# Kernel tuning notes

Hardware: AMD Instinct MI355X
Metric: run time of the kernel (lower is better)

## Reference

```python
import jax, jax.numpy as jnp
import numpy as np

N, B, C, H = 1024, 4, 1024, 8
D = C // H  # head dim = 128


def setup_inputs() -> dict:
    key = jax.random.key(0)
    ks = jax.random.split(key, 10)
    f = lambda k, s: jax.random.normal(k, s, dtype=jnp.float32)
    w = lambda k: f(k, (C, C)) * 0.02  # torch Linear weight layout (out, in)
    return {
        "query_reg": f(ks[0], (N, B, C)),
        "key_reg": f(ks[1], (N, B, C)),
        "query_cls": f(ks[2], (N, B, C)),
        "key_cls": f(ks[3], (N, B, C)),
        "value": f(ks[4], (N, B, C)),
        "W_q_reg": w(ks[5]),
        "W_k_reg": w(ks[6]),
        "W_q_cls": w(ks[7]),
        "W_k_cls": w(ks[8]),
        "W_v": w(ks[9]),
    }


def _proj_heads(x, W):
    # x: (N, B, C); torch Linear: y = x @ W.T -> reshape (N,B,H,D) -> (B,H,N,D)
    y = jnp.einsum('nbc,dc->nbd', x, W)
    return y.reshape(N, B, H, D).transpose(1, 2, 0, 3)


def _l2norm(x):
    return x / jnp.linalg.norm(x, axis=-1, keepdims=True)


def reference(query_reg, key_reg, query_cls, key_cls, value,
              W_q_reg, W_k_reg, W_q_cls, W_k_cls, W_v):
    q_reg = _l2norm(_proj_heads(query_reg, W_q_reg))  # (B,H,N,D)
    k_reg = _l2norm(_proj_heads(key_reg, W_k_reg))
    q_cls = _l2norm(_proj_heads(query_cls, W_q_cls))
    k_cls = _l2norm(_proj_heads(key_cls, W_k_cls))
    v = _proj_heads(value, W_v)

    attn_reg = jax.nn.softmax(jnp.einsum('bhnd,bhmd->bhnm', q_reg, k_reg), axis=-1)
    attn_cls = jax.nn.softmax(jnp.einsum('bhnd,bhmd->bhnm', q_cls, k_cls), axis=-1)
    attn = (attn_reg + attn_cls) * 0.5  # (B,H,N,N)

    x = jnp.einsum('bhnm,bhmd->bhnd', attn, v)  # (B,H,N,D)
    x = x.transpose(0, 2, 1, 3).reshape(B, N, C)  # (B,N,C)
    return (x.transpose(1, 0, 2), attn)  # ((N,B,C), (B,H,N,N))
```

## Files before the change

kernel.cpp:

```cpp
#include <hip/hip_runtime.h>

#define DEVINL __device__ __forceinline__

typedef unsigned short u16;
typedef float f32x4 __attribute__((ext_vector_type(4)));
typedef __bf16 bf16x8 __attribute__((ext_vector_type(8)));

constexpr int N_ = 1024, B_ = 4, C_ = 1024, H_ = 8, D_ = 128;
constexpr int NB = N_ * B_;
constexpr int BH = B_ * H_;

DEVINL u16 f2bf(float f) {
  unsigned u = __builtin_bit_cast(unsigned, f);
  u += 0x7fffu + ((u >> 16) & 1u);
  return (u16)(u >> 16);
}

typedef __attribute__((address_space(1))) void gv_t;
typedef __attribute__((address_space(3))) void lv_t;
DEVINL void gload16(const void* g, void* l) {
  __builtin_amdgcn_global_load_lds((gv_t*)(unsigned long long)g,
                                   (lv_t*)(unsigned)(unsigned long long)l, 16, 0, 0);
}
DEVINL bf16x8 ld_frag(const u16* p) { return *(const bf16x8*)p; }
DEVINL f32x4 mfma16(bf16x8 a, bf16x8 b, f32x4 c) {
  return __builtin_amdgcn_mfma_f32_16x16x32_bf16(a, b, c, 0, 0, 0);
}

struct ConvArgs { const float* s[10]; u16* d[10]; int n[10]; };

__global__ __launch_bounds__(256) void k_convert(ConvArgs a) {
  const int which = blockIdx.y;
  const int i = (blockIdx.x * 256 + threadIdx.x) * 8;
  if (i >= a.n[which]) return;
  const float* s = a.s[which] + i;
  float4 v0 = *(const float4*)s;
  float4 v1 = *(const float4*)(s + 4);
  union { uint4 v; u16 r[8]; } u;
  u.r[0] = f2bf(v0.x); u.r[1] = f2bf(v0.y); u.r[2] = f2bf(v0.z); u.r[3] = f2bf(v0.w);
  u.r[4] = f2bf(v1.x); u.r[5] = f2bf(v1.y); u.r[6] = f2bf(v1.z); u.r[7] = f2bf(v1.w);
  *(uint4*)(a.d[which] + i) = u.v;
}

struct ProjArgs { const u16* X[5]; const u16* W[5]; u16* O[5]; };

__global__ __launch_bounds__(256) void k_proj(ProjArgs a) {
  __shared__ u16 lA[128 * 64];
  __shared__ u16 lB[128 * 64];
  __shared__ float lred[128][2];
  const int tid = threadIdx.x, w = tid >> 6, lane = tid & 63;
  const int qd = lane >> 4, m16 = lane & 15;
  const int wr = w >> 1, wc = w & 1;
  const int r0 = blockIdx.y * 128, d0 = blockIdx.x * 128;
  const u16* __restrict__ X = a.X[blockIdx.z];
  const u16* __restrict__ W = a.W[blockIdx.z];
  u16* __restrict__ O = a.O[blockIdx.z];
  const bool donorm = blockIdx.z < 4;

  f32x4 acc[4][4];
  const f32x4 fz = {0.f, 0.f, 0.f, 0.f};
#pragma unroll
  for (int i = 0; i < 4; ++i)
#pragma unroll
    for (int j = 0; j < 4; ++j) acc[i][j] = fz;

  for (int k0 = 0; k0 < C_; k0 += 64) {
    __syncthreads();
#pragma unroll
    for (int i = 0; i < 4; ++i) {
      int p = i * 256 + tid, row = p >> 3, cp = p & 7, cl = cp ^ (row & 7);
      gload16(X + (size_t)(r0 + row) * C_ + k0 + cl * 8, &lA[p * 8]);
    }
#pragma unroll
    for (int i = 0; i < 4; ++i) {
      int p = i * 256 + tid, row = p >> 3, cp = p & 7, cl = cp ^ (row & 7);
      gload16(W + (size_t)(d0 + row) * C_ + k0 + cl * 8, &lB[p * 8]);
    }
    __syncthreads();
#pragma unroll
    for (int ks = 0; ks < 2; ++ks) {
      bf16x8 af[4], bfr[4];
#pragma unroll
      for (int t = 0; t < 4; ++t) {
        int row = wr * 64 + t * 16 + m16;
        af[t] = ld_frag(&lA[row * 64 + (((ks * 4 + qd) ^ (row & 7)) * 8)]);
        int col = wc * 64 + t * 16 + m16;
        bfr[t] = ld_frag(&lB[col * 64 + (((ks * 4 + qd) ^ (col & 7)) * 8)]);
      }
#pragma unroll
      for (int rt = 0; rt < 4; ++rt)
#pragma unroll
        for (int ct = 0; ct < 4; ++ct)
          acc[rt][ct] = mfma16(af[rt], bfr[ct], acc[rt][ct]);
    }
  }
  if (donorm) {
    float s[4][4];
#pragma unroll
    for (int rt = 0; rt < 4; ++rt)
#pragma unroll
      for (int rg = 0; rg < 4; ++rg) {
        float t = 0.f;
#pragma unroll
        for (int ct = 0; ct < 4; ++ct) t += acc[rt][ct][rg] * acc[rt][ct][rg];
        s[rt][rg] = t;
      }
#pragma unroll
    for (int off = 1; off < 16; off <<= 1)
#pragma unroll
      for (int rt = 0; rt < 4; ++rt)
#pragma unroll
        for (int rg = 0; rg < 4; ++rg) s[rt][rg] += __shfl_xor(s[rt][rg], off);
    if (m16 == 0) {
#pragma unroll
      for (int rt = 0; rt < 4; ++rt)
#pragma unroll
        for (int rg = 0; rg < 4; ++rg)
          lred[wr * 64 + rt * 16 + qd * 4 + rg][wc] = s[rt][rg];
    }
  }
  __syncthreads();
  float inv[4][4];
#pragma unroll
  for (int rt = 0; rt < 4; ++rt)
#pragma unroll
    for (int rg = 0; rg < 4; ++rg) {
      if (donorm) {
        int row = wr * 64 + rt * 16 + qd * 4 + rg;
        inv[rt][rg] = rsqrtf(lred[row][0] + lred[row][1]);
      } else inv[rt][rg] = 1.0f;
    }
#pragma unroll
  for (int rt = 0; rt < 4; ++rt)
#pragma unroll
    for (int ct = 0; ct < 4; ++ct)
#pragma unroll
      for (int rg = 0; rg < 4; ++rg) {
        int row = r0 + wr * 64 + rt * 16 + qd * 4 + rg;
        int col = d0 + wc * 64 + ct * 16 + m16;
        int n = row >> 2, b = row & 3, h = col >> 7, d = col & 127;
        O[(((size_t)(b * H_ + h)) * N_ + n) * D_ + d] = f2bf(acc[rt][ct][rg] * inv[rt][rg]);
      }
}

__global__ __launch_bounds__(256) void k_transpose(const u16* __restrict__ v,
                                                   u16* __restrict__ vt) {
  __shared__ u16 tile[128][65];
  const int bh = blockIdx.y, n0 = blockIdx.x * 64;
  const u16* src = v + (size_t)bh * N_ * D_;
  u16* dst = vt + (size_t)bh * D_ * N_;
  union U8 { uint4 v; u16 s[8]; };
#pragma unroll
  for (int it = 0; it < 4; ++it) {
    int c = it * 256 + threadIdx.x;
    int n = c >> 4, dc = (c & 15) * 8;
    U8 u; u.v = *(const uint4*)(src + (size_t)(n0 + n) * D_ + dc);
#pragma unroll
    for (int j = 0; j < 8; ++j) tile[dc + j][n] = u.s[j];
  }
  __syncthreads();
#pragma unroll
  for (int it = 0; it < 4; ++it) {
    int c = it * 256 + threadIdx.x;
    int d = c >> 3, nc = (c & 7) * 8;
    U8 u;
#pragma unroll
    for (int j = 0; j < 8; ++j) u.s[j] = tile[d][nc + j];
    *(uint4*)(dst + (size_t)d * N_ + n0 + nc) = u.v;
  }
}

__global__ __launch_bounds__(256, 4) void k_stats(const u16* __restrict__ qr,
                                                  const u16* __restrict__ kr,
                                                  const u16* __restrict__ qc,
                                                  const u16* __restrict__ kc,
                                                  float* __restrict__ lsum) {
  __shared__ u16 lK[128 * 128];
  __shared__ float lred[4][64];
  const int flat = blockIdx.x + (blockIdx.y << 4) + (blockIdx.z << 9);
  const int xcd = flat & 7, kk = flat >> 3;
  const int bh = (xcd << 2) + (kk >> 5);
  const int rem = kk & 31, which = rem >> 4, n0 = (rem & 15) * 64;
  const u16* Q = which ? qc : qr;
  const u16* K = which ? kc : kr;
  float* L = lsum + (size_t)which * BH * N_ + (size_t)bh * N_;
  const size_t base = (size_t)bh * N_ * D_;
  const int tid = threadIdx.x, w = tid >> 6, lane = tid & 63;
  const int qd = lane >> 4, m16 = lane & 15;

  bf16x8 qf[4][4];
#pragma unroll
  for (int ct = 0; ct < 4; ++ct)
#pragma unroll
    for (int ks = 0; ks < 4; ++ks)
      qf[ct][ks] = ld_frag(Q + base + (size_t)(n0 + ct * 16 + m16) * D_ + ks * 32 + qd * 8);

  float psum[4] = {0.f, 0.f, 0.f, 0.f};
  for (int mt = 0; mt < 8; ++mt) {
    __syncthreads();
#pragma unroll
    for (int i = 0; i < 8; ++i) {
      int p = i * 256 + tid, row = p >> 4, cp = p & 15, cl = cp ^ (row & 15);
      gload16(K + base + (size_t)(mt * 128 + row) * D_ + cl * 8, &lK[p * 8]);
    }
    __syncthreads();
#pragma unroll
    for (int rt = 0; rt < 2; ++rt) {
      bf16x8 af[4];
      const int mrow = w * 32 + rt * 16 + m16;
#pragma unroll
      for (int ks = 0; ks < 4; ++ks)
        af[ks] = ld_frag(&lK[mrow * 128 + (((ks * 4 + qd) ^ (mrow & 15)) * 8)]);
#pragma unroll
      for (int ct = 0; ct < 4; ++ct) {
        f32x4 acc = {0.f, 0.f, 0.f, 0.f};
#pragma unroll
        for (int ks = 0; ks < 4; ++ks) acc = mfma16(af[ks], qf[ct][ks], acc);
#pragma unroll
        for (int rg = 0; rg < 4; ++rg) psum[ct] += __expf(acc[rg]);
      }
    }
  }
#pragma unroll
  for (int ct = 0; ct < 4; ++ct) {
    psum[ct] += __shfl_xor(psum[ct], 16);
    psum[ct] += __shfl_xor(psum[ct], 32);
  }
  if (qd == 0) {
#pragma unroll
    for (int ct = 0; ct < 4; ++ct) lred[w][ct * 16 + m16] = psum[ct];
  }
  __syncthreads();
  if (tid < 64) L[n0 + tid] = lred[0][tid] + lred[1][tid] + lred[2][tid] + lred[3][tid];
}

__global__ __launch_bounds__(256, 3) void k_emit(const u16* __restrict__ qr,
                                                 const u16* __restrict__ kr,
                                                 const u16* __restrict__ qc,
                                                 const u16* __restrict__ kc,
                                                 const u16* __restrict__ vt,
                                                 const float* __restrict__ lsum,
                                                 float* __restrict__ out0,
                                                 float* __restrict__ out1) {
  __shared__ u16 lK[128 * 128];
  __shared__ u16 lP[32 * 136];
  const int flat = blockIdx.x + (blockIdx.y << 5);
  const int xcd = flat & 7, kk = flat >> 3;
  const int bh = (xcd << 2) + (kk >> 5);
  const int n0 = (kk & 31) * 32;
  const int b = bh >> 3, h = bh & 7;
  const size_t base = (size_t)bh * N_ * D_;
  const int tid = threadIdx.x, w = tid >> 6, lane = tid & 63;
  const int qd = lane >> 4, m16 = lane & 15;

  bf16x8 qfr[2][4], qfc[2][4];
#pragma unroll
  for (int ct = 0; ct < 2; ++ct)
#pragma unroll
    for (int ks = 0; ks < 4; ++ks) {
      size_t ro = base + (size_t)(n0 + ct * 16 + m16) * D_ + ks * 32 + qd * 8;
      qfr[ct][ks] = ld_frag(qr + ro);
      qfc[ct][ks] = ld_frag(qc + ro);
    }
  float ilr[2], ilc[2];
#pragma unroll
  for (int ct = 0; ct < 2; ++ct) {
    int n = n0 + ct * 16 + m16;
    ilr[ct] = 0.5f / lsum[(size_t)bh * N_ + n];
    ilc[ct] = 0.5f / lsum[(size_t)BH * N_ + (size_t)bh * N_ + n];
  }
  f32x4 xacc[2][2];
  const f32x4 fz = {0.f, 0.f, 0.f, 0.f};
#pragma unroll
  for (int ct = 0; ct < 2; ++ct)
#pragma unroll
    for (int dt = 0; dt < 2; ++dt) xacc[ct][dt] = fz;

  float* attn = out1 + (size_t)bh * N_ * N_;
  const u16* vtb = vt + (size_t)bh * D_ * N_;

  for (int mt = 0; mt < 8; ++mt) {
    const int m0 = mt * 128;
    f32x4 accr[2][2], accc[2][2];
    __syncthreads();
#pragma unroll
    for (int i = 0; i < 8; ++i) {
      int p = i * 256 + tid, row = p >> 4, cp = p & 15, cl = cp ^ (row & 15);
      gload16(kr + base + (size_t)(m0 + row) * D_ + cl * 8, &lK[p * 8]);
    }
    __syncthreads();
#pragma unroll
    for (int rt = 0; rt < 2; ++rt) {
      bf16x8 af[4];
      const int mrow = w * 32 + rt * 16 + m16;
#pragma unroll
      for (int ks = 0; ks < 4; ++ks)
        af[ks] = ld_frag(&lK[mrow * 128 + (((ks * 4 + qd) ^ (mrow & 15)) * 8)]);
#pragma unroll
      for (int ct = 0; ct < 2; ++ct) {
        f32x4 acc = fz;
#pragma unroll
        for (int ks = 0; ks < 4; ++ks) acc = mfma16(af[ks], qfr[ct][ks], acc);
        accr[rt][ct] = acc;
      }
    }
    __syncthreads();
#pragma unroll
    for (int i = 0; i < 8; ++i) {
      int p = i * 256 + tid, row = p >> 4, cp = p & 15, cl = cp ^ (row & 15);
      gload16(kc + base + (size_t)(m0 + row) * D_ + cl * 8, &lK[p * 8]);
    }
    __syncthreads();
#pragma unroll
    for (int rt = 0; rt < 2; ++rt) {
      bf16x8 af[4];
      const int mrow = w * 32 + rt * 16 + m16;
#pragma unroll
      for (int ks = 0; ks < 4; ++ks)
        af[ks] = ld_frag(&lK[mrow * 128 + (((ks * 4 + qd) ^ (mrow & 15)) * 8)]);
#pragma unroll
      for (int ct = 0; ct < 2; ++ct) {
        f32x4 acc = fz;
#pragma unroll
        for (int ks = 0; ks < 4; ++ks) acc = mfma16(af[ks], qfc[ct][ks], acc);
        accc[rt][ct] = acc;
      }
    }
#pragma unroll
    for (int rt = 0; rt < 2; ++rt)
#pragma unroll
      for (int ct = 0; ct < 2; ++ct) {
        f32x4 pv;
#pragma unroll
        for (int rg = 0; rg < 4; ++rg)
          pv[rg] = __expf(accr[rt][ct][rg]) * ilr[ct] + __expf(accc[rt][ct][rg]) * ilc[ct];
        const int nrow = n0 + ct * 16 + m16;
        const int mcol = m0 + w * 32 + rt * 16 + qd * 4;
        *(f32x4*)(attn + (size_t)nrow * N_ + mcol) = pv;
        union { uint2 u2; u16 s[4]; } pk;
#pragma unroll
        for (int rg = 0; rg < 4; ++rg) pk.s[rg] = f2bf(pv[rg]);
        *(uint2*)&lP[(ct * 16 + m16) * 136 + w * 32 + rt * 16 + qd * 4] = pk.u2;
      }
    __syncthreads();
#pragma unroll
    for (int ks = 0; ks < 4; ++ks) {
      bf16x8 pa[2], vb[2];
#pragma unroll
      for (int ct = 0; ct < 2; ++ct)
        pa[ct] = ld_frag(&lP[(ct * 16 + m16) * 136 + ks * 32 + qd * 8]);
#pragma unroll
      for (int dt = 0; dt < 2; ++dt)
        vb[dt] = ld_frag(vtb + (size_t)(w * 32 + dt * 16 + m16) * N_ + m0 + ks * 32 + qd * 8);
#pragma unroll
      for (int ct = 0; ct < 2; ++ct)
#pragma unroll
        for (int dt = 0; dt < 2; ++dt)
          xacc[ct][dt] = mfma16(pa[ct], vb[dt], xacc[ct][dt]);
    }
  }
#pragma unroll
  for (int ct = 0; ct < 2; ++ct)
#pragma unroll
    for (int dt = 0; dt < 2; ++dt)
#pragma unroll
      for (int rg = 0; rg < 4; ++rg) {
        int n = n0 + ct * 16 + qd * 4 + rg;
        int d = w * 32 + dt * 16 + m16;
        out0[((size_t)n * B_ + b) * C_ + h * 128 + d] = xacc[ct][dt][rg];
      }
}

extern "C" void kernel_launch(void* const* d_in, const int* in_sizes, int n_in,
                              void* d_out, int out_size, void* d_ws, size_t ws_size,
                              hipStream_t stream) {
  (void)in_sizes; (void)n_in; (void)out_size; (void)ws_size;
  const float* in_f[10];
  for (int i = 0; i < 10; ++i) in_f[i] = (const float*)d_in[i];

  u16* ws = (u16*)d_ws;
  u16* Xc[5], *Wc[5], *P[5];
  for (int i = 0; i < 5; ++i) Xc[i] = ws + (size_t)i * NB * C_;
  u16* wbase = ws + (size_t)5 * NB * C_;
  for (int i = 0; i < 5; ++i) Wc[i] = wbase + (size_t)i * C_ * C_;
  u16* pbase = wbase + (size_t)5 * C_ * C_;
  for (int i = 0; i < 5; ++i) P[i] = pbase + (size_t)i * BH * N_ * D_;
  u16* vt = pbase + (size_t)5 * BH * N_ * D_;
  float* lsum = (float*)(vt + (size_t)BH * D_ * N_);

  float* out0 = (float*)d_out;
  float* out1 = out0 + (size_t)N_ * B_ * C_;

  ConvArgs ca;
  for (int i = 0; i < 5; ++i) { ca.s[i] = in_f[i];     ca.d[i] = Xc[i];  ca.n[i] = NB * C_; }
  for (int i = 0; i < 5; ++i) { ca.s[5+i] = in_f[5+i]; ca.d[5+i] = Wc[i]; ca.n[5+i] = C_ * C_; }
  k_convert<<<dim3(2048, 10), 256, 0, stream>>>(ca);

  ProjArgs pa;
  for (int i = 0; i < 5; ++i) { pa.X[i] = Xc[i]; pa.W[i] = Wc[i]; pa.O[i] = P[i]; }
  k_proj<<<dim3(C_ / 128, NB / 128, 5), 256, 0, stream>>>(pa);

  k_transpose<<<dim3(N_ / 64, BH), 256, 0, stream>>>(P[4], vt);

  k_stats<<<dim3(N_ / 64, BH, 2), 256, 0, stream>>>(P[0], P[1], P[2], P[3], lsum);

  k_emit<<<dim3(N_ / 32, BH), 256, 0, stream>>>(P[0], P[1], P[2], P[3], vt, lsum, out0, out1);
}
```

Baseline: 412.7 us.

## Fuse softmax row-sum stats into attention kernel, caching exp scores in registers

The separate k_stats pass is removed. Each attention block now computes both QK^T score tiles once, stores exp values as packed bf16 in registers across all 8 key tiles while accumulating row sums, then normalizes and emits attn and P·V from those cached values. Both K tiles are loaded into a double-sized LDS buffer per iteration. This removes the recomputation of QK^T and the extra launch and lsum traffic, at the cost of many more registers (occupancy bound lowered to 2) and bf16 rounding of the exp values before normalization, which also changes the fp32 attn output precision.

New measurement: 411.9 us. About the same (-0.2%).

```diff
diff --git a/kernel.cpp b/kernel.cpp
--- a/kernel.cpp
+++ b/kernel.cpp
@@ -15,6 +15,7 @@
   u += 0x7fffu + ((u >> 16) & 1u);
   return (u16)(u >> 16);
 }
+DEVINL float bf2f(u16 v) { return __builtin_bit_cast(float, ((unsigned)v) << 16); }
 
 typedef __attribute__((address_space(1))) void gv_t;
 typedef __attribute__((address_space(3))) void lv_t;
@@ -170,80 +171,16 @@
   }
 }
 
-__global__ __launch_bounds__(256, 4) void k_stats(const u16* __restrict__ qr,
-                                                  const u16* __restrict__ kr,
-                                                  const u16* __restrict__ qc,
-                                                  const u16* __restrict__ kc,
-                                                  float* __restrict__ lsum) {
-  __shared__ u16 lK[128 * 128];
-  __shared__ float lred[4][64];
-  const int flat = blockIdx.x + (blockIdx.y << 4) + (blockIdx.z << 9);
-  const int xcd = flat & 7, kk = flat >> 3;
-  const int bh = (xcd << 2) + (kk >> 5);
-  const int rem = kk & 31, which = rem >> 4, n0 = (rem & 15) * 64;
-  const u16* Q = which ? qc : qr;
-  const u16* K = which ? kc : kr;
-  float* L = lsum + (size_t)which * BH * N_ + (size_t)bh * N_;
-  const size_t base = (size_t)bh * N_ * D_;
-  const int tid = threadIdx.x, w = tid >> 6, lane = tid & 63;
-  const int qd = lane >> 4, m16 = lane & 15;
-
-  bf16x8 qf[4][4];
-#pragma unroll
-  for (int ct = 0; ct < 4; ++ct)
-#pragma unroll
-    for (int ks = 0; ks < 4; ++ks)
-      qf[ct][ks] = ld_frag(Q + base + (size_t)(n0 + ct * 16 + m16) * D_ + ks * 32 + qd * 8);
-
-  float psum[4] = {0.f, 0.f, 0.f, 0.f};
-  for (int mt = 0; mt < 8; ++mt) {
-    __syncthreads();
-#pragma unroll
-    for (int i = 0; i < 8; ++i) {
-      int p = i * 256 + tid, row = p >> 4, cp = p & 15, cl = cp ^ (row & 15);
-      gload16(K + base + (size_t)(mt * 128 + row) * D_ + cl * 8, &lK[p * 8]);
-    }
-    __syncthreads();
-#pragma unroll
-    for (int rt = 0; rt < 2; ++rt) {
-      bf16x8 af[4];
-      const int mrow = w * 32 + rt * 16 + m16;
-#pragma unroll
-      for (int ks = 0; ks < 4; ++ks)
-        af[ks] = ld_frag(&lK[mrow * 128 + (((ks * 4 + qd) ^ (mrow & 15)) * 8)]);
-#pragma unroll
-      for (int ct = 0; ct < 4; ++ct) {
-        f32x4 acc = {0.f, 0.f, 0.f, 0.f};
-#pragma unroll
-        for (int ks = 0; ks < 4; ++ks) acc = mfma16(af[ks], qf[ct][ks], acc);
-#pragma unroll
-        for (int rg = 0; rg < 4; ++rg) psum[ct] += __expf(acc[rg]);
-      }
-    }
-  }
-#pragma unroll
-  for (int ct = 0; ct < 4; ++ct) {
-    psum[ct] += __shfl_xor(psum[ct], 16);
-    psum[ct] += __shfl_xor(psum[ct], 32);
-  }
-  if (qd == 0) {
-#pragma unroll
-    for (int ct = 0; ct < 4; ++ct) lred[w][ct * 16 + m16] = psum[ct];
-  }
-  __syncthreads();
-  if (tid < 64) L[n0 + tid] = lred[0][tid] + lred[1][tid] + lred[2][tid] + lred[3][tid];
-}
-
-__global__ __launch_bounds__(256, 3) void k_emit(const u16* __restrict__ qr,
+__global__ __launch_bounds__(256, 2) void k_attn(const u16* __restrict__ qr,
                                                  const u16* __restrict__ kr,
                                                  const u16* __restrict__ qc,
                                                  const u16* __restrict__ kc,
                                                  const u16* __restrict__ vt,
-                                                 const float* __restrict__ lsum,
                                                  float* __restrict__ out0,
                                                  float* __restrict__ out1) {
-  __shared__ u16 lK[128 * 128];
+  __shared__ u16 lK[2][128 * 128];
   __shared__ u16 lP[32 * 136];
+  __shared__ float lred[2][4][32];
   const int flat = blockIdx.x + (blockIdx.y << 5);
   const int xcd = flat & 7, kk = flat >> 3;
   const int bh = (xcd << 2) + (kk >> 5);
@@ -253,24 +190,88 @@
   const int tid = threadIdx.x, w = tid >> 6, lane = tid & 63;
   const int qd = lane >> 4, m16 = lane & 15;
 
-  bf16x8 qfr[2][4], qfc[2][4];
+  bf16x8 qf[2][2][4];
 #pragma unroll
   for (int ct = 0; ct < 2; ++ct)
 #pragma unroll
     for (int ks = 0; ks < 4; ++ks) {
       size_t ro = base + (size_t)(n0 + ct * 16 + m16) * D_ + ks * 32 + qd * 8;
-      qfr[ct][ks] = ld_frag(qr + ro);
-      qfc[ct][ks] = ld_frag(qc + ro);
-    }
-  float ilr[2], ilc[2];
-#pragma unroll
-  for (int ct = 0; ct < 2; ++ct) {
-    int n = n0 + ct * 16 + m16;
-    ilr[ct] = 0.5f / lsum[(size_t)bh * N_ + n];
-    ilc[ct] = 0.5f / lsum[(size_t)BH * N_ + (size_t)bh * N_ + n];
-  }
+      qf[0][ct][ks] = ld_frag(qr + ro);
+      qf[1][ct][ks] = ld_frag(qc + ro);
+    }
+
+  uint2 pst[2][8][2][2];
+  float psum[2][2] = {{0.f, 0.f}, {0.f, 0.f}};
+  const f32x4 fz = {0.f, 0.f, 0.f, 0.f};
+
+#pragma unroll
+  for (int mt = 0; mt < 8; ++mt) {
+    const int m0 = mt * 128;
+    __syncthreads();
+#pragma unroll
+    for (int i = 0; i < 8; ++i) {
+      int p = i * 256 + tid, row = p >> 4, cp = p & 15, cl = cp ^ (row & 15);
+      gload16(kr + base + (size_t)(m0 + row) * D_ + cl * 8, &lK[0][p * 8]);
+    }
+#pragma unroll
+    for (int i = 0; i < 8; ++i) {
+      int p = i * 256 + tid, row = p >> 4, cp = p & 15, cl = cp ^ (row & 15);
+      gload16(kc + base + (size_t)(m0 + row) * D_ + cl * 8, &lK[1][p * 8]);
+    }
+    __syncthreads();
+#pragma unroll
+    for (int ty = 0; ty < 2; ++ty) {
+#pragma unroll
+      for (int rt = 0; rt < 2; ++rt) {
+        bf16x8 af[4];
+        const int mrow = w * 32 + rt * 16 + m16;
+#pragma unroll
+        for (int ks = 0; ks < 4; ++ks)
+          af[ks] = ld_frag(&lK[ty][mrow * 128 + (((ks * 4 + qd) ^ (mrow & 15)) * 8)]);
+#pragma unroll
+        for (int ct = 0; ct < 2; ++ct) {
+          f32x4 acc = fz;
+#pragma unroll
+          for (int ks = 0; ks < 4; ++ks) acc = mfma16(af[ks], qf[ty][ct][ks], acc);
+          union { uint2 u; u16 s[4]; } pk;
+          float loc = 0.f;
+#pragma unroll
+          for (int rg = 0; rg < 4; ++rg) {
+            float e = __expf(acc[rg]);
+            loc += e;
+            pk.s[rg] = f2bf(e);
+          }
+          psum[ty][ct] += loc;
+          pst[ty][mt][rt][ct] = pk.u;
+        }
+      }
+    }
+  }
+
+#pragma unroll
+  for (int ty = 0; ty < 2; ++ty)
+#pragma unroll
+    for (int ct = 0; ct < 2; ++ct) {
+      psum[ty][ct] += __shfl_xor(psum[ty][ct], 16);
+      psum[ty][ct] += __shfl_xor(psum[ty][ct], 32);
+    }
+  if (qd == 0) {
+#pragma unroll
+    for (int ty = 0; ty < 2; ++ty)
+#pragma unroll
+      for (int ct = 0; ct < 2; ++ct) lred[ty][w][ct * 16 + m16] = psum[ty][ct];
+  }
+  __syncthreads();
+  float il[2][2];
+#pragma unroll
+  for (int ty = 0; ty < 2; ++ty)
+#pragma unroll
+    for (int ct = 0; ct < 2; ++ct) {
+      int n = ct * 16 + m16;
+      il[ty][ct] = 0.5f / (lred[ty][0][n] + lred[ty][1][n] + lred[ty][2][n] + lred[ty][3][n]);
+    }
+
   f32x4 xacc[2][2];
-  const f32x4 fz = {0.f, 0.f, 0.f, 0.f};
 #pragma unroll
   for (int ct = 0; ct < 2; ++ct)
 #pragma unroll
@@ -279,68 +280,27 @@
   float* attn = out1 + (size_t)bh * N_ * N_;
   const u16* vtb = vt + (size_t)bh * D_ * N_;
 
+#pragma unroll
   for (int mt = 0; mt < 8; ++mt) {
     const int m0 = mt * 128;
-    f32x4 accr[2][2], accc[2][2];
-    __syncthreads();
-#pragma unroll
-    for (int i = 0; i < 8; ++i) {
-      int p = i * 256 + tid, row = p >> 4, cp = p & 15, cl = cp ^ (row & 15);
-      gload16(kr + base + (size_t)(m0 + row) * D_ + cl * 8, &lK[p * 8]);
-    }
-    __syncthreads();
-#pragma unroll
-    for (int rt = 0; rt < 2; ++rt) {
-      bf16x8 af[4];
-      const int mrow = w * 32 + rt * 16 + m16;
-#pragma unroll
-      for (int ks = 0; ks < 4; ++ks)
-        af[ks] = ld_frag(&lK[mrow * 128 + (((ks * 4 + qd) ^ (mrow & 15)) * 8)]);
+    __syncthreads();
+#pragma unroll
+    for (int rt = 0; rt < 2; ++rt)
 #pragma unroll
       for (int ct = 0; ct < 2; ++ct) {
-        f32x4 acc = fz;
-#pragma unroll
-        for (int ks = 0; ks < 4; ++ks) acc = mfma16(af[ks], qfr[ct][ks], acc);
-        accr[rt][ct] = acc;
-      }
-    }
-    __syncthreads();
-#pragma unroll
-    for (int i = 0; i < 8; ++i) {
-      int p = i * 256 + tid, row = p >> 4, cp = p & 15, cl = cp ^ (row & 15);
-      gload16(kc + base + (size_t)(m0 + row) * D_ + cl * 8, &lK[p * 8]);
-    }
-    __syncthreads();
-#pragma unroll
-    for (int rt = 0; rt < 2; ++rt) {
-      bf16x8 af[4];
-      const int mrow = w * 32 + rt * 16 + m16;
-#pragma unroll
-      for (int ks = 0; ks < 4; ++ks)
-        af[ks] = ld_frag(&lK[mrow * 128 + (((ks * 4 + qd) ^ (mrow & 15)) * 8)]);
-#pragma unroll
-      for (int ct = 0; ct < 2; ++ct) {
-        f32x4 acc = fz;
-#pragma unroll
-        for (int ks = 0; ks < 4; ++ks) acc = mfma16(af[ks], qfc[ct][ks], acc);
-        accc[rt][ct] = acc;
-      }
-    }
-#pragma unroll
-    for (int rt = 0; rt < 2; ++rt)
-#pragma unroll
-      for (int ct = 0; ct < 2; ++ct) {
+        union { uint2 u; u16 s[4]; } ur, uc, pk;
+        ur.u = pst[0][mt][rt][ct];
+        uc.u = pst[1][mt][rt][ct];
         f32x4 pv;
 #pragma unroll
-        for (int rg = 0; rg < 4; ++rg)
-          pv[rg] = __expf(accr[rt][ct][rg]) * ilr[ct] + __expf(accc[rt][ct][rg]) * ilc[ct];
+        for (int rg = 0; rg < 4; ++rg) {
+          pv[rg] = bf2f(ur.s[rg]) * il[0][ct] + bf2f(uc.s[rg]) * il[1][ct];
+          pk.s[rg] = f2bf(pv[rg]);
+        }
         const int nrow = n0 + ct * 16 + m16;
         const int mcol = m0 + w * 32 + rt * 16 + qd * 4;
         *(f32x4*)(attn + (size_t)nrow * N_ + mcol) = pv;
-        union { uint2 u2; u16 s[4]; } pk;
-#pragma unroll
-        for (int rg = 0; rg < 4; ++rg) pk.s[rg] = f2bf(pv[rg]);
-        *(uint2*)&lP[(ct * 16 + m16) * 136 + w * 32 + rt * 16 + qd * 4] = pk.u2;
+        *(uint2*)&lP[(ct * 16 + m16) * 136 + w * 32 + rt * 16 + qd * 4] = pk.u;
       }
     __syncthreads();
 #pragma unroll
@@ -386,7 +346,6 @@
   u16* pbase = wbase + (size_t)5 * C_ * C_;
   for (int i = 0; i < 5; ++i) P[i] = pbase + (size_t)i * BH * N_ * D_;
   u16* vt = pbase + (size_t)5 * BH * N_ * D_;
-  float* lsum = (float*)(vt + (size_t)BH * D_ * N_);
 
   float* out0 = (float*)d_out;
   float* out1 = out0 + (size_t)N_ * B_ * C_;
@@ -402,7 +361,5 @@
 
   k_transpose<<<dim3(N_ / 64, BH), 256, 0, stream>>>(P[4], vt);
 
-  k_stats<<<dim3(N_ / 64, BH, 2), 256, 0, stream>>>(P[0], P[1], P[2], P[3], lsum);
-
-  k_emit<<<dim3(N_ / 32, BH), 256, 0, stream>>>(P[0], P[1], P[2], P[3], vt, lsum, out0, out1);
-}
+  k_attn<<<dim3(N_ / 32, BH), 256, 0, stream>>>(P[0], P[1], P[2], P[3], vt, out0, out1);
+}
```
